# Optimization experiments

Hardware: AMD Instinct MI355X
Metric: run time of the kernel (lower is better)

Reference implementation:

```python
import jax, jax.numpy as jnp
import numpy as np

N_NODES = 100000
N_EDGES = 50000   # number of hyperedges
NNZ = 500000      # incidence entries
IN_C = 128
OUT_C = 128


def setup_inputs() -> dict:
    key = jax.random.key(0)
    k1, k2, k3, k4 = jax.random.split(key, 4)
    x = jax.random.normal(k1, (N_NODES, IN_C), dtype=jnp.float32)
    node_idx = jax.random.randint(k2, (NNZ,), 0, N_NODES, dtype=jnp.int32)
    edge_idx = jax.random.randint(k3, (NNZ,), 0, N_EDGES, dtype=jnp.int32)
    hyperedge_index = jnp.stack([node_idx, edge_idx], axis=0)  # [2, NNZ]
    W = jax.random.normal(k4, (IN_C, OUT_C), dtype=jnp.float32) / np.sqrt(IN_C).astype(np.float32)
    b = jnp.zeros((OUT_C,), dtype=jnp.float32)
    return {"x": x, "hyperedge_index": hyperedge_index, "W": W, "b": b}


def reference(x, hyperedge_index, W, b):
    # PyG HypergraphConv (use_attention=False, heads=1, unit hyperedge weights):
    #   out = D^{-1} H B^{-1} H^T (X W) + b
    node_idx = hyperedge_index[0]  # [NNZ] node index of each incidence
    edge_idx = hyperedge_index[1]  # [NNZ] hyperedge index of each incidence

    xw = x @ W  # [N_NODES, OUT_C]

    ones = jnp.ones(node_idx.shape[0], dtype=xw.dtype)
    deg_n = jax.ops.segment_sum(ones, node_idx, num_segments=N_NODES)  # D
    d_inv = jnp.where(deg_n > 0, 1.0 / deg_n, 0.0)
    deg_e = jax.ops.segment_sum(ones, edge_idx, num_segments=N_EDGES)  # B
    b_inv = jnp.where(deg_e > 0, 1.0 / deg_e, 0.0)

    # node -> hyperedge: m_e = B^{-1}_e * sum_{v in e} xw_v
    edge_feat = jax.ops.segment_sum(xw[node_idx], edge_idx, num_segments=N_EDGES)
    edge_feat = edge_feat * b_inv[:, None]  # [N_EDGES, OUT_C]

    # hyperedge -> node: out_v = D^{-1}_v * sum_{e \ni v} m_e
    out = jax.ops.segment_sum(edge_feat[edge_idx], node_idx, num_segments=N_NODES)
    out = out * d_inv[:, None]  # [N_NODES, OUT_C]

    return out + b
```

## Files before the change

kernel.cpp:

```cpp
#include <hip/hip_runtime.h>

typedef unsigned short u16;
typedef unsigned int u32;

#define N_NODES 100000
#define N_EDGES 50000
#define C 128
#define NCNT (N_EDGES + N_NODES)
#define NBUCKC 1172
#define BCHUNK 2048

static __device__ __forceinline__ float bf2f(u16 h) {
    u32 u = ((u32)h) << 16;
    float f;
    __builtin_memcpy(&f, &u, 4);
    return f;
}

static __device__ __forceinline__ u16 f2bf(float f) {
    u32 u;
    __builtin_memcpy(&u, &f, 4);
    return (u16)((u + 0x7fffu + ((u >> 16) & 1u)) >> 16);
}

typedef short s16x8 __attribute__((ext_vector_type(8)));
typedef float f32x4 __attribute__((ext_vector_type(4)));

__global__ __launch_bounds__(256) void prep_k(
    const float* __restrict__ W, u16* __restrict__ Wt,
    const int* __restrict__ ni, const int* __restrict__ ei,
    u32* __restrict__ cntM, int nnz, int nb1) {
    __shared__ u32 h[NBUCKC];
    if (blockIdx.x < 64) {
        int idx = blockIdx.x * 256 + threadIdx.x;
        int k = idx >> 7, oc = idx & 127;
        Wt[oc * 128 + k] = f2bf(W[k * 128 + oc]);
        return;
    }
    int blk = blockIdx.x - 64;
    for (int b = threadIdx.x; b < NBUCKC; b += 256) h[b] = 0;
    __syncthreads();
    int i0 = blk * BCHUNK;
    int iend = min(i0 + BCHUNK, nnz);
    for (int i = i0 + threadIdx.x; i < iend; i += 256) {
        int e = ei[i], n = ni[i];
        atomicAdd(&h[e >> 7], 1u);
        atomicAdd(&h[(N_EDGES + n) >> 7], 1u);
    }
    __syncthreads();
    for (int b = threadIdx.x; b < NBUCKC; b += 256)
        cntM[(size_t)b * nb1 + blk] = h[b];
}

__global__ __launch_bounds__(256) void scan_a2(const u32* __restrict__ cnt,
                                               u32* __restrict__ off,
                                               u32* __restrict__ bsum, int N) {
    __shared__ u32 wsum[4];
    int tid = threadIdx.x;
    int base = blockIdx.x * 1024 + tid * 4;
    u32 v0 = 0, v1 = 0, v2 = 0, v3 = 0;
    if (base + 3 < N) {
        uint4 v = *(const uint4*)(cnt + base);
        v0 = v.x; v1 = v.y; v2 = v.z; v3 = v.w;
    } else {
        if (base + 0 < N) v0 = cnt[base + 0];
        if (base + 1 < N) v1 = cnt[base + 1];
        if (base + 2 < N) v2 = cnt[base + 2];
        if (base + 3 < N) v3 = cnt[base + 3];
    }
    u32 s = v0 + v1 + v2 + v3;
    int lane = tid & 63, wv = tid >> 6;
    u32 x = s;
    for (int d = 1; d < 64; d <<= 1) {
        u32 y = __shfl_up(x, (unsigned)d);
        if (lane >= d) x += y;
    }
    if (lane == 63) wsum[wv] = x;
    __syncthreads();
    u32 wo = 0;
    for (int w = 0; w < 4; ++w) wo += (w < wv) ? wsum[w] : 0u;
    u32 ex = wo + x - s;
    if (base + 0 < N) off[base + 0] = ex;
    if (base + 1 < N) off[base + 1] = ex + v0;
    if (base + 2 < N) off[base + 2] = ex + v0 + v1;
    if (base + 3 < N) off[base + 3] = ex + v0 + v1 + v2;
    if (tid == 255) bsum[blockIdx.x] = wo + x;
}

__global__ __launch_bounds__(256) void scan_b2(u32* __restrict__ bsum, int nb) {
    __shared__ u32 wsum[4];
    int t = threadIdx.x;
    u32 v0 = (2 * t < nb) ? bsum[2 * t] : 0u;
    u32 v1 = (2 * t + 1 < nb) ? bsum[2 * t + 1] : 0u;
    u32 s = v0 + v1;
    int lane = t & 63, wv = t >> 6;
    u32 x = s;
    for (int d = 1; d < 64; d <<= 1) {
        u32 y = __shfl_up(x, (unsigned)d);
        if (lane >= d) x += y;
    }
    if (lane == 63) wsum[wv] = x;
    __syncthreads();
    u32 wo = 0;
    for (int w = 0; w < 4; ++w) wo += (w < wv) ? wsum[w] : 0u;
    u32 ex = wo + x - s;
    if (2 * t < nb) bsum[2 * t] = ex;
    if (2 * t + 1 < nb) bsum[2 * t + 1] = ex + v0;
}

__global__ __launch_bounds__(256) void bucket_place_k(
    const int* __restrict__ ni, const int* __restrict__ ei,
    const u32* __restrict__ offM, const u32* __restrict__ bsum,
    u32* __restrict__ stage, int nnz, int nb1) {
    __shared__ u32 cur[NBUCKC];
    for (int b = threadIdx.x; b < NBUCKC; b += 256) {
        size_t idx = (size_t)b * nb1 + blockIdx.x;
        cur[b] = offM[idx] + bsum[idx >> 10];
    }
    __syncthreads();
    int i0 = blockIdx.x * BCHUNK;
    int iend = min(i0 + BCHUNK, nnz);
    for (int i = i0 + threadIdx.x; i < iend; i += 256) {
        int e = ei[i], n = ni[i];
        u32 p1 = atomicAdd(&cur[e >> 7], 1u);
        stage[p1] = ((u32)(e & 127) << 17) | (u32)n;
        int k2 = N_EDGES + n;
        u32 p2 = atomicAdd(&cur[k2 >> 7], 1u);
        stage[p2] = ((u32)(k2 & 127) << 17) | (u32)e;
    }
}

__global__ __launch_bounds__(256) void bucket_csr_k(
    const u32* __restrict__ offM, const u32* __restrict__ bsum,
    const u32* __restrict__ stage, u32* __restrict__ csr,
    uint2* __restrict__ rowinfo, int nnz, int nb1) {
    __shared__ u32 h[128];
    __shared__ u32 ks[128];
    int b = blockIdx.x;
    size_t i0 = (size_t)b * nb1;
    u32 gstart = offM[i0] + bsum[i0 >> 10];
    u32 gend;
    if (b + 1 < NBUCKC) {
        size_t i1 = (size_t)(b + 1) * nb1;
        gend = offM[i1] + bsum[i1 >> 10];
    } else {
        gend = (u32)(2 * nnz);
    }
    int size = (int)(gend - gstart);
    if (threadIdx.x < 128) h[threadIdx.x] = 0;
    __syncthreads();
    for (int i = threadIdx.x; i < size; i += 256)
        atomicAdd(&h[stage[gstart + i] >> 17], 1u);
    __syncthreads();
    if (threadIdx.x < 64) {
        int l = threadIdx.x;
        u32 s0 = h[2 * l], s1 = h[2 * l + 1];
        u32 ps = s0 + s1;
        u32 x = ps;
        for (int d = 1; d < 64; d <<= 1) {
            u32 y = __shfl_up(x, (unsigned)d);
            if (l >= d) x += y;
        }
        u32 ex = x - ps;
        ks[2 * l] = ex;
        ks[2 * l + 1] = ex + s0;
        int gk = b * 128 + 2 * l;
        if (gk < NCNT) rowinfo[gk] = make_uint2(gstart + ex, s0);
        if (gk + 1 < NCNT) rowinfo[gk + 1] = make_uint2(gstart + ex + s0, s1);
    }
    __syncthreads();
    for (int i = threadIdx.x; i < size; i += 256) {
        u32 en = stage[gstart + i];
        u32 kl = en >> 17;
        u32 p = atomicAdd(&ks[kl], 1u);
        csr[gstart + p] = en & 0x1FFFFu;
    }
}

__global__ __launch_bounds__(256) void edge_gather_x(const float* __restrict__ x,
                                                     const uint2* __restrict__ rowinfo,
                                                     const u32* __restrict__ csrC,
                                                     u16* __restrict__ G) {
    int e = blockIdx.x * 4 + (threadIdx.x >> 6);
    if (e >= N_EDGES) return;
    int lane = threadIdx.x & 63;
    int half = lane >> 5, ch = lane & 31;
    uint2 ri = rowinfo[e];
    u32 deg = ri.y;
    u32 start = ri.x;
    float a0 = 0.f, a1 = 0.f, a2 = 0.f, a3 = 0.f;
    for (u32 base = 0; base < deg; base += 64) {
        int m = (int)min(64u, deg - base);
        int myidx = (lane < m) ? (int)csrC[start + base + lane] : 0;
        for (int t = 0; t < m; t += 8) {
            int e0 = min(t + 0 + half, m - 1), e1 = min(t + 2 + half, m - 1);
            int e2 = min(t + 4 + half, m - 1), e3 = min(t + 6 + half, m - 1);
            int r0 = __shfl(myidx, e0), r1 = __shfl(myidx, e1);
            int r2 = __shfl(myidx, e2), r3 = __shfl(myidx, e3);
            float4 v0 = ((const float4*)(x + (size_t)r0 * C))[ch];
            float4 v1 = ((const float4*)(x + (size_t)r1 * C))[ch];
            float4 v2 = ((const float4*)(x + (size_t)r2 * C))[ch];
            float4 v3 = ((const float4*)(x + (size_t)r3 * C))[ch];
            float m0 = (t + 0 + half < m) ? 1.f : 0.f;
            float m1 = (t + 2 + half < m) ? 1.f : 0.f;
            float m2 = (t + 4 + half < m) ? 1.f : 0.f;
            float m3 = (t + 6 + half < m) ? 1.f : 0.f;
            a0 += m0 * v0.x + m1 * v1.x + m2 * v2.x + m3 * v3.x;
            a1 += m0 * v0.y + m1 * v1.y + m2 * v2.y + m3 * v3.y;
            a2 += m0 * v0.z + m1 * v1.z + m2 * v2.z + m3 * v3.z;
            a3 += m0 * v0.w + m1 * v1.w + m2 * v2.w + m3 * v3.w;
        }
    }
    a0 += __shfl_xor(a0, 32);
    a1 += __shfl_xor(a1, 32);
    a2 += __shfl_xor(a2, 32);
    a3 += __shfl_xor(a3, 32);
    float sc = deg ? 1.f / (float)deg : 0.f;
    if (lane < 32) {
        uint2 w;
        w.x = (u32)f2bf(a0 * sc) | ((u32)f2bf(a1 * sc) << 16);
        w.y = (u32)f2bf(a2 * sc) | ((u32)f2bf(a3 * sc) << 16);
        ((uint2*)(G + (size_t)e * C))[ch] = w;
    }
}

__global__ __launch_bounds__(256) void gemm_e(
    const u16* __restrict__ G, const u16* __restrict__ Wt,
    u16* __restrict__ ef) {
    int wave = threadIdx.x >> 6;
    int tile = blockIdx.x * 4 + wave;
    if (tile >= 3125) return;
    int lane = threadIdx.x & 63;
    int m = lane & 15;
    int quad = lane >> 4;
    int row0 = tile * 16;

    const u16* gr = G + (size_t)(row0 + m) * C + quad * 8;
    union { uint4 u; s16x8 v; } a[4];
#pragma unroll
    for (int kk = 0; kk < 4; ++kk)
        a[kk].u = *(const uint4*)(gr + kk * 32);

    f32x4 acc[8];
#pragma unroll
    for (int nt = 0; nt < 8; ++nt) acc[nt] = (f32x4){0.f, 0.f, 0.f, 0.f};

#pragma unroll
    for (int kk = 0; kk < 4; ++kk) {
        int kb = kk * 32 + quad * 8;
#pragma unroll
        for (int nt = 0; nt < 8; ++nt) {
            union { uint4 u; s16x8 v; } b;
            b.u = *(const uint4*)(Wt + (size_t)(nt * 16 + m) * C + kb);
            acc[nt] = __builtin_amdgcn_mfma_f32_16x16x32_bf16(a[kk].v, b.v, acc[nt], 0, 0, 0);
        }
    }

#pragma unroll
    for (int nt = 0; nt < 8; ++nt) {
#pragma unroll
        for (int r = 0; r < 4; ++r) {
            int row = row0 + quad * 4 + r;
            ef[(size_t)row * C + nt * 16 + m] = f2bf(acc[nt][r]);
        }
    }
}

__global__ __launch_bounds__(256) void node_gather_k(const u16* __restrict__ ef,
                                                     const uint2* __restrict__ rowinfo,
                                                     const u32* __restrict__ csrC,
                                                     const float* __restrict__ bias,
                                                     float* __restrict__ out) {
    int v = blockIdx.x * 4 + (threadIdx.x >> 6);
    if (v >= N_NODES) return;
    int lane = threadIdx.x & 63;
    int half = lane >> 5, ch = lane & 31;
    uint2 ri = rowinfo[N_EDGES + v];
    u32 deg = ri.y;
    u32 start = ri.x;
    float a0 = 0.f, a1 = 0.f, a2 = 0.f, a3 = 0.f;
    for (u32 base = 0; base < deg; base += 64) {
        int m = (int)min(64u, deg - base);
        int myidx = (lane < m) ? (int)csrC[start + base + lane] : 0;
        for (int t = 0; t < m; t += 8) {
            int e0 = min(t + 0 + half, m - 1), e1 = min(t + 2 + half, m - 1);
            int e2 = min(t + 4 + half, m - 1), e3 = min(t + 6 + half, m - 1);
            int r0 = __shfl(myidx, e0), r1 = __shfl(myidx, e1);
            int r2 = __shfl(myidx, e2), r3 = __shfl(myidx, e3);
            uint2 u0 = ((const uint2*)(ef + (size_t)r0 * C))[ch];
            uint2 u1 = ((const uint2*)(ef + (size_t)r1 * C))[ch];
            uint2 u2 = ((const uint2*)(ef + (size_t)r2 * C))[ch];
            uint2 u3 = ((const uint2*)(ef + (size_t)r3 * C))[ch];
            float m0 = (t + 0 + half < m) ? 1.f : 0.f;
            float m1 = (t + 2 + half < m) ? 1.f : 0.f;
            float m2 = (t + 4 + half < m) ? 1.f : 0.f;
            float m3 = (t + 6 + half < m) ? 1.f : 0.f;
            a0 += m0 * bf2f((u16)(u0.x & 0xffffu)) + m1 * bf2f((u16)(u1.x & 0xffffu))
                + m2 * bf2f((u16)(u2.x & 0xffffu)) + m3 * bf2f((u16)(u3.x & 0xffffu));
            a1 += m0 * bf2f((u16)(u0.x >> 16)) + m1 * bf2f((u16)(u1.x >> 16))
                + m2 * bf2f((u16)(u2.x >> 16)) + m3 * bf2f((u16)(u3.x >> 16));
            a2 += m0 * bf2f((u16)(u0.y & 0xffffu)) + m1 * bf2f((u16)(u1.y & 0xffffu))
                + m2 * bf2f((u16)(u2.y & 0xffffu)) + m3 * bf2f((u16)(u3.y & 0xffffu));
            a3 += m0 * bf2f((u16)(u0.y >> 16)) + m1 * bf2f((u16)(u1.y >> 16))
                + m2 * bf2f((u16)(u2.y >> 16)) + m3 * bf2f((u16)(u3.y >> 16));
        }
    }
    a0 += __shfl_xor(a0, 32);
    a1 += __shfl_xor(a1, 32);
    a2 += __shfl_xor(a2, 32);
    a3 += __shfl_xor(a3, 32);
    float sc = deg ? 1.f / (float)deg : 0.f;
    if (lane < 32) {
        float4 bv = *(const float4*)(bias + ch * 4);
        float4 w;
        w.x = a0 * sc + bv.x;
        w.y = a1 * sc + bv.y;
        w.z = a2 * sc + bv.z;
        w.w = a3 * sc + bv.w;
        ((float4*)(out + (size_t)v * C))[ch] = w;
    }
}

extern "C" void kernel_launch(void* const* d_in, const int* in_sizes, int n_in,
                              void* d_out, int out_size, void* d_ws, size_t ws_size,
                              hipStream_t stream) {
    const float* x = (const float*)d_in[0];
    const int* node_idx = (const int*)d_in[1];
    const int nnz = in_sizes[1] / 2;
    const int* edge_idx = node_idx + nnz;
    const float* W = (const float*)d_in[2];
    const float* bias = (const float*)d_in[3];
    float* out = (float*)d_out;

    int nb1 = (nnz + BCHUNK - 1) / BCHUNK;
    int scanN = NBUCKC * nb1;
    int scanBlocks = (scanN + 1023) / 1024;

    u16* Wt = (u16*)d_ws;
    u16* ef = Wt + 16384;
    u32* cntM = (u32*)(ef + (size_t)N_EDGES * C);
    u32* offM = cntM + scanN;
    u32* bsum2 = offM + scanN;
    uint2* rowinfo = (uint2*)(bsum2 + 512);
    u32* csrC = (u32*)(rowinfo + NCNT);

    u16* G = (u16*)d_out;
    u32* stage = (u32*)((char*)d_out + (size_t)N_NODES * C * 2);

    prep_k<<<64 + nb1, 256, 0, stream>>>(W, Wt, node_idx, edge_idx, cntM, nnz, nb1);
    scan_a2<<<scanBlocks, 256, 0, stream>>>(cntM, offM, bsum2, scanN);
    scan_b2<<<1, 256, 0, stream>>>(bsum2, scanBlocks);
    bucket_place_k<<<nb1, 256, 0, stream>>>(node_idx, edge_idx, offM, bsum2,
                                            stage, nnz, nb1);
    bucket_csr_k<<<NBUCKC, 256, 0, stream>>>(offM, bsum2, stage, csrC, rowinfo,
                                             nnz, nb1);
    edge_gather_x<<<(N_EDGES + 3) / 4, 256, 0, stream>>>(x, rowinfo, csrC, G);
    gemm_e<<<(3125 + 3) / 4, 256, 0, stream>>>(G, Wt, ef);
    node_gather_k<<<(N_NODES + 3) / 4, 256, 0, stream>>>(ef, rowinfo, csrC, bias, out);
}
```

Before: 208.5 us.

## Fuse edge gather and edge GEMM into one kernel via shared-memory tile

Merges the hyperedge feature gather and the bf16 MFMA projection into a single kernel. Each block gathers 16 hyperedges into a padded LDS tile, then its four waves each compute two 16-column output tiles. This removes the global round trip of the intermediate G buffer and one kernel launch. In exchange each wave processes four edges serially before a block barrier, which may reduce latency hiding in the gather phase.

```diff
diff --git a/kernel.cpp b/kernel.cpp
--- a/kernel.cpp
+++ b/kernel.cpp
@@ -9,6 +9,7 @@
 #define NCNT (N_EDGES + N_NODES)
 #define NBUCKC 1172
 #define BCHUNK 2048
+#define GSTRIDE 136
 
 static __device__ __forceinline__ float bf2f(u16 h) {
     u32 u = ((u32)h) << 16;
@@ -177,92 +178,87 @@
     }
 }
 
-__global__ __launch_bounds__(256) void edge_gather_x(const float* __restrict__ x,
-                                                     const uint2* __restrict__ rowinfo,
-                                                     const u32* __restrict__ csrC,
-                                                     u16* __restrict__ G) {
-    int e = blockIdx.x * 4 + (threadIdx.x >> 6);
-    if (e >= N_EDGES) return;
+__global__ __launch_bounds__(256) void edge_gemm_k(
+    const float* __restrict__ x, const uint2* __restrict__ rowinfo,
+    const u32* __restrict__ csrC, const u16* __restrict__ Wt,
+    u16* __restrict__ ef) {
+    __shared__ __align__(16) u16 gs[16 * GSTRIDE];
     int lane = threadIdx.x & 63;
+    int wave = threadIdx.x >> 6;
     int half = lane >> 5, ch = lane & 31;
-    uint2 ri = rowinfo[e];
-    u32 deg = ri.y;
-    u32 start = ri.x;
-    float a0 = 0.f, a1 = 0.f, a2 = 0.f, a3 = 0.f;
-    for (u32 base = 0; base < deg; base += 64) {
-        int m = (int)min(64u, deg - base);
-        int myidx = (lane < m) ? (int)csrC[start + base + lane] : 0;
-        for (int t = 0; t < m; t += 8) {
-            int e0 = min(t + 0 + half, m - 1), e1 = min(t + 2 + half, m - 1);
-            int e2 = min(t + 4 + half, m - 1), e3 = min(t + 6 + half, m - 1);
-            int r0 = __shfl(myidx, e0), r1 = __shfl(myidx, e1);
-            int r2 = __shfl(myidx, e2), r3 = __shfl(myidx, e3);
-            float4 v0 = ((const float4*)(x + (size_t)r0 * C))[ch];
-            float4 v1 = ((const float4*)(x + (size_t)r1 * C))[ch];
-            float4 v2 = ((const float4*)(x + (size_t)r2 * C))[ch];
-            float4 v3 = ((const float4*)(x + (size_t)r3 * C))[ch];
-            float m0 = (t + 0 + half < m) ? 1.f : 0.f;
-            float m1 = (t + 2 + half < m) ? 1.f : 0.f;
-            float m2 = (t + 4 + half < m) ? 1.f : 0.f;
-            float m3 = (t + 6 + half < m) ? 1.f : 0.f;
-            a0 += m0 * v0.x + m1 * v1.x + m2 * v2.x + m3 * v3.x;
-            a1 += m0 * v0.y + m1 * v1.y + m2 * v2.y + m3 * v3.y;
-            a2 += m0 * v0.z + m1 * v1.z + m2 * v2.z + m3 * v3.z;
-            a3 += m0 * v0.w + m1 * v1.w + m2 * v2.w + m3 * v3.w;
-        }
-    }
-    a0 += __shfl_xor(a0, 32);
-    a1 += __shfl_xor(a1, 32);
-    a2 += __shfl_xor(a2, 32);
-    a3 += __shfl_xor(a3, 32);
-    float sc = deg ? 1.f / (float)deg : 0.f;
-    if (lane < 32) {
-        uint2 w;
-        w.x = (u32)f2bf(a0 * sc) | ((u32)f2bf(a1 * sc) << 16);
-        w.y = (u32)f2bf(a2 * sc) | ((u32)f2bf(a3 * sc) << 16);
-        ((uint2*)(G + (size_t)e * C))[ch] = w;
-    }
-}
-
-__global__ __launch_bounds__(256) void gemm_e(
-    const u16* __restrict__ G, const u16* __restrict__ Wt,
-    u16* __restrict__ ef) {
-    int wave = threadIdx.x >> 6;
-    int tile = blockIdx.x * 4 + wave;
-    if (tile >= 3125) return;
-    int lane = threadIdx.x & 63;
+    int ebase = blockIdx.x * 16;
+
+#pragma unroll
+    for (int s = 0; s < 4; ++s) {
+        int row = wave + s * 4;
+        int e = ebase + row;
+        uint2 ri = rowinfo[e];
+        u32 deg = ri.y;
+        u32 start = ri.x;
+        float a0 = 0.f, a1 = 0.f, a2 = 0.f, a3 = 0.f;
+        for (u32 base = 0; base < deg; base += 64) {
+            int m = (int)min(64u, deg - base);
+            int myidx = (lane < m) ? (int)csrC[start + base + lane] : 0;
+            for (int t = 0; t < m; t += 8) {
+                int e0 = min(t + 0 + half, m - 1), e1 = min(t + 2 + half, m - 1);
+                int e2 = min(t + 4 + half, m - 1), e3 = min(t + 6 + half, m - 1);
+                int r0 = __shfl(myidx, e0), r1 = __shfl(myidx, e1);
+                int r2 = __shfl(myidx, e2), r3 = __shfl(myidx, e3);
+                float4 v0 = ((const float4*)(x + (size_t)r0 * C))[ch];
+                float4 v1 = ((const float4*)(x + (size_t)r1 * C))[ch];
+                float4 v2 = ((const float4*)(x + (size_t)r2 * C))[ch];
+                float4 v3 = ((const float4*)(x + (size_t)r3 * C))[ch];
+                float m0 = (t + 0 + half < m) ? 1.f : 0.f;
+                float m1 = (t + 2 + half < m) ? 1.f : 0.f;
+                float m2 = (t + 4 + half < m) ? 1.f : 0.f;
+                float m3 = (t + 6 + half < m) ? 1.f : 0.f;
+                a0 += m0 * v0.x + m1 * v1.x + m2 * v2.x + m3 * v3.x;
+                a1 += m0 * v0.y + m1 * v1.y + m2 * v2.y + m3 * v3.y;
+                a2 += m0 * v0.z + m1 * v1.z + m2 * v2.z + m3 * v3.z;
+                a3 += m0 * v0.w + m1 * v1.w + m2 * v2.w + m3 * v3.w;
+            }
+        }
+        a0 += __shfl_xor(a0, 32);
+        a1 += __shfl_xor(a1, 32);
+        a2 += __shfl_xor(a2, 32);
+        a3 += __shfl_xor(a3, 32);
+        float sc = deg ? 1.f / (float)deg : 0.f;
+        if (lane < 32) {
+            uint2 w;
+            w.x = (u32)f2bf(a0 * sc) | ((u32)f2bf(a1 * sc) << 16);
+            w.y = (u32)f2bf(a2 * sc) | ((u32)f2bf(a3 * sc) << 16);
+            *(uint2*)(&gs[row * GSTRIDE + ch * 4]) = w;
+        }
+    }
+    __syncthreads();
+
     int m = lane & 15;
     int quad = lane >> 4;
-    int row0 = tile * 16;
-
-    const u16* gr = G + (size_t)(row0 + m) * C + quad * 8;
     union { uint4 u; s16x8 v; } a[4];
 #pragma unroll
     for (int kk = 0; kk < 4; ++kk)
-        a[kk].u = *(const uint4*)(gr + kk * 32);
-
-    f32x4 acc[8];
-#pragma unroll
-    for (int nt = 0; nt < 8; ++nt) acc[nt] = (f32x4){0.f, 0.f, 0.f, 0.f};
-
+        a[kk].u = *(const uint4*)(&gs[m * GSTRIDE + quad * 8 + kk * 32]);
+
+    f32x4 acc[2];
+    acc[0] = (f32x4){0.f, 0.f, 0.f, 0.f};
+    acc[1] = (f32x4){0.f, 0.f, 0.f, 0.f};
 #pragma unroll
     for (int kk = 0; kk < 4; ++kk) {
         int kb = kk * 32 + quad * 8;
 #pragma unroll
-        for (int nt = 0; nt < 8; ++nt) {
+        for (int j = 0; j < 2; ++j) {
+            int nt = wave * 2 + j;
             union { uint4 u; s16x8 v; } b;
             b.u = *(const uint4*)(Wt + (size_t)(nt * 16 + m) * C + kb);
-            acc[nt] = __builtin_amdgcn_mfma_f32_16x16x32_bf16(a[kk].v, b.v, acc[nt], 0, 0, 0);
-        }
-    }
-
-#pragma unroll
-    for (int nt = 0; nt < 8; ++nt) {
-#pragma unroll
-        for (int r = 0; r < 4; ++r) {
-            int row = row0 + quad * 4 + r;
-            ef[(size_t)row * C + nt * 16 + m] = f2bf(acc[nt][r]);
-        }
+            acc[j] = __builtin_amdgcn_mfma_f32_16x16x32_bf16(a[kk].v, b.v, acc[j], 0, 0, 0);
+        }
+    }
+#pragma unroll
+    for (int j = 0; j < 2; ++j) {
+        int nt = wave * 2 + j;
+#pragma unroll
+        for (int r = 0; r < 4; ++r)
+            ef[(size_t)(ebase + quad * 4 + r) * C + nt * 16 + m] = f2bf(acc[j][r]);
     }
 }
 
@@ -344,7 +340,6 @@
     uint2* rowinfo = (uint2*)(bsum2 + 512);
     u32* csrC = (u32*)(rowinfo + NCNT);
 
-    u16* G = (u16*)d_out;
     u32* stage = (u32*)((char*)d_out + (size_t)N_NODES * C * 2);
 
     prep_k<<<64 + nb1, 256, 0, stream>>>(W, Wt, node_idx, edge_idx, cntM, nnz, nb1);
@@ -354,7 +349,6 @@
                                             stage, nnz, nb1);
     bucket_csr_k<<<NBUCKC, 256, 0, stream>>>(offM, bsum2, stage, csrC, rowinfo,
                                              nnz, nb1);
-    edge_gather_x<<<(N_EDGES + 3) / 4, 256, 0, stream>>>(x, rowinfo, csrC, G);
-    gemm_e<<<(3125 + 3) / 4, 256, 0, stream>>>(G, Wt, ef);
+    edge_gemm_k<<<N_EDGES / 16, 256, 0, stream>>>(x, rowinfo, csrC, Wt, ef);
     node_gather_k<<<(N_NODES + 3) / 4, 256, 0, stream>>>(ef, rowinfo, csrC, bias, out);
 }
```

Result: faster. 197.3 us (-5.3%).
